# Kernel optimization log

Measured on AMD Instinct MI355X. Metric: run time of the kernel, lower is better.

The kernel has to match this reference:

```python
import jax, jax.numpy as jnp
import numpy as np

DIM = 1024
NUM_HEADS = 16
HEAD_DIM = DIM // NUM_HEADS
SCALE = HEAD_DIM ** -0.5


def setup_inputs() -> dict:
    key = jax.random.key(0)
    k_x, k_wq, k_bq, k_wp, k_bp = jax.random.split(key, 5)
    x = jax.random.normal(k_x, (2, 2048, DIM), dtype=jnp.float32)
    # torch Linear weights: [out_features, in_features]
    W_qkv = jax.random.normal(k_wq, (3 * DIM, DIM), dtype=jnp.float32) * (DIM ** -0.5)
    b_qkv = jax.random.normal(k_bq, (3 * DIM,), dtype=jnp.float32) * 0.02
    W_proj = jax.random.normal(k_wp, (DIM, DIM), dtype=jnp.float32) * (DIM ** -0.5)
    b_proj = jax.random.normal(k_bp, (DIM,), dtype=jnp.float32) * 0.02
    return {"x": x, "W_qkv": W_qkv, "b_qkv": b_qkv, "W_proj": W_proj, "b_proj": b_proj}


def reference(x, W_qkv, b_qkv, W_proj, b_proj):
    B, N, C = x.shape
    qkv = x @ W_qkv.T + b_qkv                      # [B, N, 3C]
    q, k, v = jnp.split(qkv, 3, axis=-1)           # each [B, N, C]
    def heads(t):
        return t.reshape(B, N, NUM_HEADS, HEAD_DIM).transpose(0, 2, 1, 3)  # [B,H,N,D]
    q, k, v = heads(q), heads(k), heads(v)
    attn = jnp.einsum('bhnd,bhmd->bhnm', q, k) * SCALE
    attn = jax.nn.softmax(attn, axis=-1)
    out = jnp.einsum('bhnm,bhmd->bhnd', attn, v)   # [B,H,N,D]
    out = out.transpose(0, 2, 1, 3).reshape(B, N, C)
    return out @ W_proj.T + b_proj
```

## Files before the change

kernel.cpp:

```cpp
#include <hip/hip_runtime.h>


typedef unsigned short u16;
typedef __attribute__((ext_vector_type(8))) _Float16 f16x8;
typedef __attribute__((ext_vector_type(4))) float f32x4;

#define DEV static __device__ __forceinline__
#define MFMA16(a, b, c) __builtin_amdgcn_mfma_f32_16x16x32_f16(a, b, c, 0, 0, 0)

DEV u16 f2h(float f) { _Float16 h = (_Float16)f; return __builtin_bit_cast(u16, h); }
DEV float h2f(u16 u) { return (float)__builtin_bit_cast(_Float16, u); }
DEV unsigned pack_h2(float a, float b) {
  return (unsigned)f2h(a) | ((unsigned)f2h(b) << 16);
}

DEV void async16(u16* dst, const u16* src) {
  __builtin_amdgcn_global_load_lds(
      (const __attribute__((address_space(1))) unsigned int*)(const void*)src,
      (__attribute__((address_space(3))) unsigned int*)(void*)dst, 16, 0, 0);
}

__global__ __launch_bounds__(256) void k_split_all(
    const float* __restrict__ x, const float* __restrict__ wq,
    const float* __restrict__ wp, u16* __restrict__ xh,
    u16* __restrict__ wqh, u16* __restrict__ wph) {
  int i = blockIdx.x * 256 + threadIdx.x;
  const float* src;
  u16* dh;
  int off;
  if (i < 1048576) { src = x;  dh = xh;  off = i; }
  else if (i < 1835008) { src = wq; dh = wqh; off = i - 1048576; }
  else { src = wp; dh = wph; off = i - 1835008; }
  float4 v = ((const float4*)src)[off];
  ushort4 h;
  h.x = f2h(v.x); h.y = f2h(v.y); h.z = f2h(v.z); h.w = f2h(v.w);
  ((ushort4*)dh)[off] = h;
}

template <int MODE>
__global__ __launch_bounds__(512) void k_gemm(
    const u16* __restrict__ Ah_g, const u16* __restrict__ Bh_g,
    const float* __restrict__ bias,
    u16* __restrict__ oQh, u16* __restrict__ oKh, u16* __restrict__ oVh,
    float* __restrict__ fout, int nbn) {
  __shared__ u16 lds[32768];
  const int t = threadIdx.x;
  const int lane = t & 63, g = lane >> 4, cl = lane & 15;
  const int w = t >> 6;
  const int mi = blockIdx.x / nbn, ni = blockIdx.x % nbn;
  const int m0 = mi * 128, n0 = ni * 128;
  const int wr = (w >> 1) * 32, wc = (w & 1) * 64;

  f32x4 acc[2][4] = {};

#define STAGE_AB(kt_, pb_)                                                  \
  {                                                                         \
    const int k0__ = (kt_) * 64;                                            \
    const unsigned pb__ = (pb_);                                            \
    _Pragma("unroll") for (int j = 0; j < 4; ++j) {                         \
      int gs = j * 512 + t;                                                 \
      int tensor = gs >> 10;                                                \
      int s = gs & 1023;                                                    \
      int row = s >> 3;                                                     \
      int c = (s & 7) ^ (row & 7);                                          \
      const u16* src = tensor ? Bh_g + (n0 + row) * 1024 + k0__ + c * 8     \
                              : Ah_g + (m0 + row) * 1024 + k0__ + c * 8;    \
      async16(&lds[pb__ + (unsigned)(gs & ~63) * 8], src);                  \
    }                                                                       \
  }

#define COMPUTE_TILE(base_)                                                 \
  {                                                                         \
    const unsigned base__ = (base_);                                        \
    _Pragma("unroll") for (int ks = 0; ks < 2; ++ks) {                      \
      f16x8 af[2], bfr[4];                                                  \
      _Pragma("unroll") for (int fm = 0; fm < 2; ++fm) {                    \
        int rowL = wr + fm * 16 + cl;                                       \
        unsigned idx = base__ + rowL * 64 + (((4 * ks + g) ^ (rowL & 7)) * 8); \
        af[fm] = *(const f16x8*)&lds[idx];                                  \
      }                                                                     \
      _Pragma("unroll") for (int fn = 0; fn < 4; ++fn) {                    \
        int rowL = wc + fn * 16 + cl;                                       \
        unsigned idx = base__ + 8192 + rowL * 64 +                          \
                       (((4 * ks + g) ^ (rowL & 7)) * 8);                   \
        bfr[fn] = *(const f16x8*)&lds[idx];                                 \
      }                                                                     \
      _Pragma("unroll") for (int fm = 0; fm < 2; ++fm)                      \
        _Pragma("unroll") for (int fn = 0; fn < 4; ++fn)                    \
          acc[fm][fn] = MFMA16(af[fm], bfr[fn], acc[fm][fn]);               \
    }                                                                       \
  }

  STAGE_AB(0, 0u);
  STAGE_AB(1, 16384u);

  for (int kt = 0; kt < 15; ++kt) {
    asm volatile("s_waitcnt vmcnt(4)" ::: "memory");
    __builtin_amdgcn_sched_barrier(0);
    __builtin_amdgcn_s_barrier();
    __builtin_amdgcn_sched_barrier(0);
    const unsigned base = (kt & 1) ? 16384u : 0u;
    COMPUTE_TILE(base);
    asm volatile("s_waitcnt lgkmcnt(0)" ::: "memory");
    __builtin_amdgcn_sched_barrier(0);
    __builtin_amdgcn_s_barrier();
    __builtin_amdgcn_sched_barrier(0);
    if (kt < 14) STAGE_AB(kt + 2, base);
  }
  asm volatile("s_waitcnt vmcnt(0)" ::: "memory");
  __builtin_amdgcn_sched_barrier(0);
  __builtin_amdgcn_s_barrier();
  __builtin_amdgcn_sched_barrier(0);
  COMPUTE_TILE(16384u);
#undef STAGE_AB
#undef COMPUTE_TILE

#pragma unroll
  for (int fm = 0; fm < 2; ++fm) {
#pragma unroll
    for (int fn = 0; fn < 4; ++fn) {
      int cc = n0 + wc + fn * 16 + cl;
      float bv = bias[cc];
      f32x4 a = acc[fm][fn];
#pragma unroll
      for (int r = 0; r < 4; ++r) {
        int rr = m0 + wr + fm * 16 + g * 4 + r;
        float v = a[r] + bv;
        if (MODE == 0) {
          int seg = cc >> 10, cm = cc & 1023;
          int h = cm >> 6, d = cm & 63;
          int b = rr >> 11, n = rr & 2047;
          int bh = b * 16 + h;
          if (seg == 0) {
            v *= 0.1803368801111204f;
            oQh[(bh * 2048 + n) * 64 + d] = f2h(v);
          } else if (seg == 1) {
            oKh[(bh * 2048 + n) * 64 + d] = f2h(v);
          } else {
            oVh[(bh * 64 + d) * 2048 + n] = f2h(v);
          }
        } else {
          fout[rr * 1024 + cc] = v;
        }
      }
    }
  }
}

__global__ __launch_bounds__(512, 4) void k_attn(
    const u16* __restrict__ Qh, const u16* __restrict__ Kh,
    const u16* __restrict__ Vh, u16* __restrict__ Oh) {
  __shared__ u16 lds[24576];
  const int t = threadIdx.x, w = t >> 6, lane = t & 63, g = lane >> 4, cl = lane & 15;
  int bid = (blockIdx.x & 7) * 64 + (blockIdx.x >> 3);
  const int bh = bid >> 4, qt = bid & 15;
  const int n0 = qt * 128;
  const int PH = 16384 + w * 1024;

  f16x8 qf[2];
  {
    int rg = bh * 2048 + n0 + w * 16 + cl;
#pragma unroll
    for (int ks = 0; ks < 2; ++ks)
      qf[ks] = *(const f16x8*)&Qh[rg * 64 + ks * 32 + g * 8];
  }

  f32x4 o[4] = {};
  f32x4 ps4 = {0.f, 0.f, 0.f, 0.f};
  const int bsrc = (lane & 48) | ((lane >> 2) & 12);
  const int swz = (cl & 7) << 3;

#define STAGE_KV(kt_, pbase_)                                              \
  {                                                                        \
    const int kt__ = (kt_);                                                \
    const unsigned pb__ = (pbase_);                                        \
    _Pragma("unroll") for (int j = 0; j < 2; ++j) {                        \
      int gs = j * 512 + t;                                                \
      int tensor = gs >> 9, s = gs & 511, row = s >> 3;                    \
      int c = (s & 7) ^ (row & 7);                                         \
      const u16* src;                                                      \
      if (tensor == 0)                                                     \
        src = Kh + (bh * 2048 + kt__ * 64 + row) * 64 + c * 8;             \
      else                                                                 \
        src = Vh + (bh * 64 + row) * 2048 + kt__ * 64 + c * 8;             \
      async16(&lds[pb__ + (unsigned)(gs & ~63) * 8], src);                 \
    }                                                                      \
  }

  STAGE_KV(0, 0u);
  __syncthreads();
  unsigned p = 0;

  for (int kt = 0; kt < 32; ++kt) {
    const unsigned base = p * 8192u;
    if (kt < 31) STAGE_KV(kt + 1, base ^ 8192u);

    f32x4 st[4] = {};
    __builtin_amdgcn_s_setprio(1);
#pragma unroll
    for (int fn = 0; fn < 4; ++fn) {
      int krow = fn * 16 + cl;
#pragma unroll
      for (int ks = 0; ks < 2; ++ks) {
        unsigned idx = base + krow * 64 + (((4 * ks + g) ^ (krow & 7)) * 8);
        f16x8 kf = *(const f16x8*)&lds[idx];
        st[fn] = MFMA16(kf, qf[ks], st[fn]);
      }
    }
    __builtin_amdgcn_s_setprio(0);

    unsigned upk[4][2];
#pragma unroll
    for (int fn = 0; fn < 4; ++fn) {
      float p0 = __builtin_amdgcn_exp2f(st[fn][0]);
      float p1 = __builtin_amdgcn_exp2f(st[fn][1]);
      float p2 = __builtin_amdgcn_exp2f(st[fn][2]);
      float p3 = __builtin_amdgcn_exp2f(st[fn][3]);
      ps4[0] += p0; ps4[1] += p1; ps4[2] += p2; ps4[3] += p3;
      upk[fn][0] = pack_h2(p0, p1);
      upk[fn][1] = pack_h2(p2, p3);
    }

#pragma unroll
    for (int fn = 0; fn < 4; ++fn) {
      int addr = (cl * 64 + fn * 16 + 4 * g) ^ swz;
      *(uint2*)&lds[PH + addr] = make_uint2(upk[fn][0], upk[fn][1]);
    }

    f16x8 pa[2];
#pragma unroll
    for (int ks = 0; ks < 2; ++ks) {
      int addr = (cl * 64 + ks * 32 + 8 * g) ^ swz;
      pa[ks] = *(const f16x8*)&lds[PH + addr];
    }

    __builtin_amdgcn_s_setprio(1);
#pragma unroll
    for (int fd = 0; fd < 4; ++fd) {
      int vrow = fd * 16 + cl;
#pragma unroll
      for (int ks = 0; ks < 2; ++ks) {
        unsigned idx = base + 4096 + vrow * 64 + (((4 * ks + g) ^ (vrow & 7)) * 8);
        f16x8 vf = *(const f16x8*)&lds[idx];
        o[fd] = MFMA16(pa[ks], vf, o[fd]);
      }
    }
    __builtin_amdgcn_s_setprio(0);
    __syncthreads();
    p ^= 1;
  }
#undef STAGE_KV

  float lrun = (ps4[0] + ps4[1]) + (ps4[2] + ps4[3]);
  lrun += __shfl_xor(lrun, 16);
  lrun += __shfl_xor(lrun, 32);
  const int b = bh >> 4, h = bh & 15;
  float l0 = __shfl(lrun, bsrc), l1 = __shfl(lrun, bsrc | 1);
  float l2 = __shfl(lrun, bsrc | 2), l3 = __shfl(lrun, bsrc | 3);
  float inv[4] = {1.0f / l0, 1.0f / l1, 1.0f / l2, 1.0f / l3};
#pragma unroll
  for (int fd = 0; fd < 4; ++fd)
#pragma unroll
    for (int r = 0; r < 4; ++r) {
      float v = o[fd][r] * inv[r];
      int rowg = b * 2048 + n0 + w * 16 + 4 * g + r;
      int colg = h * 64 + fd * 16 + cl;
      Oh[rowg * 1024 + colg] = f2h(v);
    }
}

extern "C" void kernel_launch(void* const* d_in, const int* in_sizes, int n_in,
                              void* d_out, int out_size, void* d_ws, size_t ws_size,
                              hipStream_t stream) {
  const float* x  = (const float*)d_in[0];
  const float* Wq = (const float*)d_in[1];
  const float* bq = (const float*)d_in[2];
  const float* Wp = (const float*)d_in[3];
  const float* bp = (const float*)d_in[4];
  float* out = (float*)d_out;
  char* ws = (char*)d_ws;

  u16* Xh  = (u16*)(ws + 0);
  u16* Wqh = (u16*)(ws + 8388608);
  u16* Wph = (u16*)(ws + 14680064);
  u16* Qh  = (u16*)(ws + 16777216);
  u16* Kh  = (u16*)(ws + 25165824);
  u16* Vh  = (u16*)(ws + 33554432);

  k_split_all<<<8192, 256, 0, stream>>>(x, Wq, Wp, Xh, Wqh, Wph);

  k_gemm<0><<<32 * 24, 512, 0, stream>>>(Xh, Wqh, bq, Qh, Kh, Vh, nullptr, 24);
  k_attn<<<512, 512, 0, stream>>>(Qh, Kh, Vh, Xh);
  k_gemm<1><<<32 * 8, 512, 0, stream>>>(Xh, Wph, bp,
                                        nullptr, nullptr, nullptr, out, 8);
}
```

Measured before the change: 126.3 us.

## Deepen KV prefetch to two tiles ahead with explicit vmcnt waits

Restructures the attention KV loop so that two tiles are in flight. Each iteration waits only until the current tile's loads are done (vmcnt(2)), and the next-next tile is issued after the compute barrier, replacing the old scheme of one prefetch per iteration followed by a full __syncthreads. It also swaps the two scalar fp16 conversions for the packed cvt_pkrtz instruction, which rounds toward zero instead of to nearest. The aim is to hide global-to-LDS latency and cut conversion instructions, at the cost of hand-placed waitcnt and barrier handling that must exactly match the in-flight load counts.

```diff
diff --git a/kernel.cpp b/kernel.cpp
--- a/kernel.cpp
+++ b/kernel.cpp
@@ -3,6 +3,7 @@
 
 typedef unsigned short u16;
 typedef __attribute__((ext_vector_type(8))) _Float16 f16x8;
+typedef __attribute__((ext_vector_type(2))) __fp16 fp16x2;
 typedef __attribute__((ext_vector_type(4))) float f32x4;
 
 #define DEV static __device__ __forceinline__
@@ -10,8 +11,9 @@
 
 DEV u16 f2h(float f) { _Float16 h = (_Float16)f; return __builtin_bit_cast(u16, h); }
 DEV float h2f(u16 u) { return (float)__builtin_bit_cast(_Float16, u); }
-DEV unsigned pack_h2(float a, float b) {
-  return (unsigned)f2h(a) | ((unsigned)f2h(b) << 16);
+DEV unsigned pkrtz(float a, float b) {
+  fp16x2 h2 = __builtin_amdgcn_cvt_pkrtz(a, b);
+  return __builtin_bit_cast(unsigned, h2);
 }
 
 DEV void async16(u16* dst, const u16* src) {
@@ -187,69 +189,75 @@
     }                                                                      \
   }
 
+#define COMPUTE_KV(base_)                                                   \
+  {                                                                         \
+    const unsigned base__ = (base_);                                        \
+    f32x4 st[4] = {};                                                       \
+    __builtin_amdgcn_s_setprio(1);                                          \
+    _Pragma("unroll") for (int fn = 0; fn < 4; ++fn) {                      \
+      int krow = fn * 16 + cl;                                              \
+      _Pragma("unroll") for (int ks = 0; ks < 2; ++ks) {                    \
+        unsigned idx = base__ + krow * 64 + (((4 * ks + g) ^ (krow & 7)) * 8); \
+        f16x8 kf = *(const f16x8*)&lds[idx];                                \
+        st[fn] = MFMA16(kf, qf[ks], st[fn]);                                \
+      }                                                                     \
+    }                                                                       \
+    __builtin_amdgcn_s_setprio(0);                                          \
+    unsigned upk[4][2];                                                     \
+    _Pragma("unroll") for (int fn = 0; fn < 4; ++fn) {                      \
+      float p0 = __builtin_amdgcn_exp2f(st[fn][0]);                         \
+      float p1 = __builtin_amdgcn_exp2f(st[fn][1]);                         \
+      float p2 = __builtin_amdgcn_exp2f(st[fn][2]);                         \
+      float p3 = __builtin_amdgcn_exp2f(st[fn][3]);                         \
+      ps4[0] += p0; ps4[1] += p1; ps4[2] += p2; ps4[3] += p3;               \
+      upk[fn][0] = pkrtz(p0, p1);                                           \
+      upk[fn][1] = pkrtz(p2, p3);                                           \
+    }                                                                       \
+    _Pragma("unroll") for (int fn = 0; fn < 4; ++fn) {                      \
+      int addr = (cl * 64 + fn * 16 + 4 * g) ^ swz;                         \
+      *(uint2*)&lds[PH + addr] = make_uint2(upk[fn][0], upk[fn][1]);        \
+    }                                                                       \
+    f16x8 pa[2];                                                            \
+    _Pragma("unroll") for (int ks = 0; ks < 2; ++ks) {                      \
+      int addr = (cl * 64 + ks * 32 + 8 * g) ^ swz;                         \
+      pa[ks] = *(const f16x8*)&lds[PH + addr];                              \
+    }                                                                       \
+    __builtin_amdgcn_s_setprio(1);                                          \
+    _Pragma("unroll") for (int fd = 0; fd < 4; ++fd) {                      \
+      int vrow = fd * 16 + cl;                                              \
+      _Pragma("unroll") for (int ks = 0; ks < 2; ++ks) {                    \
+        unsigned idx = base__ + 4096 + vrow * 64 +                          \
+                       (((4 * ks + g) ^ (vrow & 7)) * 8);                   \
+        f16x8 vf = *(const f16x8*)&lds[idx];                                \
+        o[fd] = MFMA16(pa[ks], vf, o[fd]);                                  \
+      }                                                                     \
+    }                                                                       \
+    __builtin_amdgcn_s_setprio(0);                                          \
+  }
+
   STAGE_KV(0, 0u);
-  __syncthreads();
-  unsigned p = 0;
-
-  for (int kt = 0; kt < 32; ++kt) {
-    const unsigned base = p * 8192u;
-    if (kt < 31) STAGE_KV(kt + 1, base ^ 8192u);
-
-    f32x4 st[4] = {};
-    __builtin_amdgcn_s_setprio(1);
-#pragma unroll
-    for (int fn = 0; fn < 4; ++fn) {
-      int krow = fn * 16 + cl;
-#pragma unroll
-      for (int ks = 0; ks < 2; ++ks) {
-        unsigned idx = base + krow * 64 + (((4 * ks + g) ^ (krow & 7)) * 8);
-        f16x8 kf = *(const f16x8*)&lds[idx];
-        st[fn] = MFMA16(kf, qf[ks], st[fn]);
-      }
-    }
-    __builtin_amdgcn_s_setprio(0);
-
-    unsigned upk[4][2];
-#pragma unroll
-    for (int fn = 0; fn < 4; ++fn) {
-      float p0 = __builtin_amdgcn_exp2f(st[fn][0]);
-      float p1 = __builtin_amdgcn_exp2f(st[fn][1]);
-      float p2 = __builtin_amdgcn_exp2f(st[fn][2]);
-      float p3 = __builtin_amdgcn_exp2f(st[fn][3]);
-      ps4[0] += p0; ps4[1] += p1; ps4[2] += p2; ps4[3] += p3;
-      upk[fn][0] = pack_h2(p0, p1);
-      upk[fn][1] = pack_h2(p2, p3);
-    }
-
-#pragma unroll
-    for (int fn = 0; fn < 4; ++fn) {
-      int addr = (cl * 64 + fn * 16 + 4 * g) ^ swz;
-      *(uint2*)&lds[PH + addr] = make_uint2(upk[fn][0], upk[fn][1]);
-    }
-
-    f16x8 pa[2];
-#pragma unroll
-    for (int ks = 0; ks < 2; ++ks) {
-      int addr = (cl * 64 + ks * 32 + 8 * g) ^ swz;
-      pa[ks] = *(const f16x8*)&lds[PH + addr];
-    }
-
-    __builtin_amdgcn_s_setprio(1);
-#pragma unroll
-    for (int fd = 0; fd < 4; ++fd) {
-      int vrow = fd * 16 + cl;
-#pragma unroll
-      for (int ks = 0; ks < 2; ++ks) {
-        unsigned idx = base + 4096 + vrow * 64 + (((4 * ks + g) ^ (vrow & 7)) * 8);
-        f16x8 vf = *(const f16x8*)&lds[idx];
-        o[fd] = MFMA16(pa[ks], vf, o[fd]);
-      }
-    }
-    __builtin_amdgcn_s_setprio(0);
-    __syncthreads();
-    p ^= 1;
-  }
+  STAGE_KV(1, 8192u);
+
+  for (int kt = 0; kt < 31; ++kt) {
+    asm volatile("s_waitcnt vmcnt(2)" ::: "memory");
+    __builtin_amdgcn_sched_barrier(0);
+    __builtin_amdgcn_s_barrier();
+    __builtin_amdgcn_sched_barrier(0);
+    const unsigned base = (kt & 1) ? 8192u : 0u;
+    COMPUTE_KV(base);
+    asm volatile("s_waitcnt lgkmcnt(0)" ::: "memory");
+    __builtin_amdgcn_sched_barrier(0);
+    __builtin_amdgcn_s_barrier();
+    __builtin_amdgcn_sched_barrier(0);
+    if (kt < 30) STAGE_KV(kt + 2, base);
+  }
+  asm volatile("s_waitcnt vmcnt(0)" ::: "memory");
+  __builtin_amdgcn_sched_barrier(0);
+  __builtin_amdgcn_s_barrier();
+  __builtin_amdgcn_sched_barrier(0);
+  COMPUTE_KV(8192u);
 #undef STAGE_KV
+#undef COMPUTE_KV
 
   float lrun = (ps4[0] + ps4[1]) + (ps4[2] + ps4[3]);
   lrun += __shfl_xor(lrun, 16);
```

After: 123.8 us. 1.02x faster.
